# Performance work log

Hardware: AMD Instinct MI355X
Metric: run time of the kernel (lower is better)

## Reference

```python
import jax, jax.numpy as jnp
import numpy as np

B, S, V, NC, CV, CE, WE, KS = 64, 256, 50000, 20, 256, 32, 512, 4


def setup_inputs() -> dict:
    key = jax.random.key(0)
    k1, k2, k3, k4 = jax.random.split(key, 4)
    data = jax.random.randint(k1, (B, S), 0, V, dtype=jnp.int32)
    spelling = jax.random.randint(k2, (V, NC), 0, CV, dtype=jnp.int32)
    char_emb_w = jax.random.normal(k3, (CV, CE), dtype=jnp.float32)
    cnn_w = jax.random.uniform(k4, (WE, CE + 1, KS), dtype=jnp.float32,
                               minval=-0.05, maxval=0.05)
    return {"char_emb_w": char_emb_w, "cnn_w": cnn_w,
            "data": data, "spelling": spelling}


def reference(char_emb_w, cnn_w, data, spelling):
    # spelling gather: [B,S] -> [B,S,NC] char ids -> [B,S,NC,CE] char embeddings
    sp = spelling[data]
    ce = char_emb_w[sp]
    bsz, seq_len, nc, ces = ce.shape
    x = ce.reshape(bsz * seq_len, nc, ces)
    # mode='l2' -> lang bit is 1.0 (would be 0.0 for 'l1')
    lang_bit = jnp.ones((bsz * seq_len, nc, 1), dtype=x.dtype)
    x = jnp.concatenate([x, lang_bit], axis=2).transpose(0, 2, 1)  # [N, CE+1, NC]
    # Conv1d, valid padding, no bias: [N, WE, NC-KS+1]
    y = jax.lax.conv_general_dilated(x, cnn_w, window_strides=(1,),
                                     padding='VALID',
                                     dimension_numbers=('NCH', 'OIH', 'NCH'))
    # MaxPool1d over full remaining length
    word_emb = jnp.max(y, axis=2)  # [N, WE]
    return word_emb.reshape(bsz, seq_len, -1)
```

## Files before the change

### kernel.cpp

```cpp
#include <hip/hip_runtime.h>
#include <hip/hip_bf16.h>
#include <cstdint>

#define NWORDS 16384
#define NCH    20
#define CEDIM  32
#define WEDIM  512
#define WPB    16
#define NBLK   (NWORDS/WPB)

#define AS3 __attribute__((address_space(3)))
#define AS1 __attribute__((address_space(1)))

typedef __attribute__((ext_vector_type(8))) short bf16x8;
typedef __attribute__((ext_vector_type(4))) float f32x4;

__device__ __forceinline__ unsigned short f2bf(float f){
    union { float f; unsigned int u; } v; v.f = f;
    unsigned int u = v.u + 0x7fffu + ((v.u >> 16) & 1u);
    return (unsigned short)(u >> 16);
}

__global__ __launch_bounds__(256) void prep_kernel(const float* __restrict__ cnn,
                                                   const float* __restrict__ cemb,
                                                   unsigned short* __restrict__ wbf2,
                                                   unsigned short* __restrict__ cembbf,
                                                   float* __restrict__ bias){
    int idx = blockIdx.x * 256 + threadIdx.x;
    if (idx < 65536){
        int j  = idx & 7;
        int col= (idx >> 3) & 63;
        int kc = (idx >> 9) & 15;
        int cc = idx >> 13;
        int o  = cc*64 + col;
        int kk = kc*8 + j;
        int i  = kk & 31, k = kk >> 5;
        wbf2[idx] = f2bf(cnn[o*132 + i*4 + k]);
    } else if (idx < 65536 + 257*CEDIM){
        int r = idx - 65536;
        cembbf[r] = (r < 256*CEDIM) ? f2bf(cemb[r]) : (unsigned short)0;
    } else if (idx < 65536 + 257*CEDIM + WEDIM){
        int o = idx - (65536 + 257*CEDIM);
        const float* p = cnn + o*132 + 128;
        bias[o] = p[0] + p[1] + p[2] + p[3];
    }
}

__global__ __attribute__((amdgpu_waves_per_eu(2,2))) __launch_bounds__(256)
void conv_kernel(
    const int* __restrict__ data,
    const int* __restrict__ spelling,
    const unsigned short* __restrict__ cembbf,
    const unsigned short* __restrict__ wbf2,
    const float* __restrict__ bias,
    float* __restrict__ out)
{
    __shared__ __align__(16) unsigned short sW[2][8192];
    __shared__ int scid[WPB*NCH];

    const int tid   = threadIdx.x;
    const int wv    = tid >> 6;
    const int lane  = tid & 63;
    const int lr    = lane & 15, lq = lane >> 4;
    const int wbase = blockIdx.x * WPB;

    {
        const unsigned short* gp0 = wbf2;
        #pragma unroll
        for (int t = 0; t < 4; ++t){
            int slot = wv*4 + t;
            const unsigned short* gp = gp0 + slot*512 + lane*8;
            unsigned short* lp = &sW[0][slot*512];
            __builtin_amdgcn_global_load_lds((const AS1 void*)gp, (AS3 void*)lp, 16, 0, 0);
        }
    }
    for (int s = tid; s < WPB*NCH; s += 256){
        int w = s / NCH, j = s - w*NCH;
        scid[s] = spelling[data[wbase + w]*NCH + j];
    }
    __syncthreads();

    const char* cb = (const char*)cembbf;
    const int lqoff = lq * 16;

    bf16x8 af[4][4];
    #pragma unroll
    for (int mi = 0; mi < 4; ++mi){
        const int* sp = &scid[(wv*4 + mi)*NCH + lr];
        #pragma unroll
        for (int q = 0; q < 4; ++q)
            af[mi][q] = *reinterpret_cast<const bf16x8*>(cb + sp[q]*64 + lqoff);
    }
    bf16x8 axf[4];
    #pragma unroll
    for (int q = 0; q < 4; ++q){
        int ch = (lr < 4) ? scid[(wv*4 + lr)*NCH + 16 + q] : 256;
        axf[q] = *reinterpret_cast<const bf16x8*>(cb + ch*64 + lqoff);
    }

    const float* biasl = bias + lane;

    #pragma unroll 1
    for (int cc = 0; cc < 8; ++cc){
        const int cur = cc & 1, nxt = cur ^ 1;

        if (cc < 7){
            const unsigned short* gp0 = wbf2 + (cc+1)*8192;
            #pragma unroll
            for (int t = 0; t < 4; ++t){
                int slot = wv*4 + t;
                const unsigned short* gp = gp0 + slot*512 + lane*8;
                unsigned short* lp = &sW[nxt][slot*512];
                __builtin_amdgcn_global_load_lds((const AS1 void*)gp, (AS3 void*)lp, 16, 0, 0);
            }
        }

        f32x4 acc[4][4], accX[4];
        {
            f32x4 z = {0.f, 0.f, 0.f, 0.f};
            #pragma unroll
            for (int ni = 0; ni < 4; ++ni){
                accX[ni] = z;
                #pragma unroll
                for (int mi = 0; mi < 4; ++mi) acc[mi][ni] = z;
            }
        }

        #pragma unroll
        for (int q = 0; q < 4; ++q){
            const unsigned short* wl = &sW[cur][(q*4 + lq)*512 + lr*8];
            bf16x8 bb[4];
            #pragma unroll
            for (int ni = 0; ni < 4; ++ni)
                bb[ni] = *reinterpret_cast<const bf16x8*>(wl + ni*128);
            #pragma unroll
            for (int ni = 0; ni < 4; ++ni){
                #pragma unroll
                for (int mi = 0; mi < 4; ++mi)
                    acc[mi][ni] = __builtin_amdgcn_mfma_f32_16x16x32_bf16(
                        af[mi][q], bb[ni], acc[mi][ni], 0, 0, 0);
                accX[ni] = __builtin_amdgcn_mfma_f32_16x16x32_bf16(
                        axf[q], bb[ni], accX[ni], 0, 0, 0);
            }
        }

        float bv = biasl[cc*64];
        #pragma unroll
        for (int mi = 0; mi < 4; ++mi){
            float mred[4];
            #pragma unroll
            for (int ni = 0; ni < 4; ++ni){
                float m = fmaxf(fmaxf(acc[mi][ni][0], acc[mi][ni][1]),
                                fmaxf(acc[mi][ni][2], acc[mi][ni][3]));
                if (lq == 0) m = fmaxf(m, accX[ni][mi]);
                m = fmaxf(m, __shfl_xor(m, 16, 64));
                m = fmaxf(m, __shfl_xor(m, 32, 64));
                mred[ni] = m;
            }
            float mv = (lq == 0) ? mred[0] : (lq == 1) ? mred[1]
                     : (lq == 2) ? mred[2] : mred[3];
            __builtin_nontemporal_store(
                mv + bv, &out[(wbase + wv*4 + mi)*WEDIM + cc*64 + lane]);
        }

        __syncthreads();
    }
}

extern "C" void kernel_launch(void* const* d_in, const int* in_sizes, int n_in,
                              void* d_out, int out_size, void* d_ws, size_t ws_size,
                              hipStream_t stream) {
    const float* cemb     = (const float*)d_in[0];
    const float* cnn      = (const float*)d_in[1];
    const int*   data     = (const int*)d_in[2];
    const int*   spelling = (const int*)d_in[3];
    float* outp = (float*)d_out;

    unsigned short* wbf2   = (unsigned short*)d_ws;
    float*          bias   = (float*)((char*)d_ws + 131072);
    unsigned short* cembbf = (unsigned short*)((char*)d_ws + 133120);

    int prep_items = 65536 + 257*CEDIM + WEDIM;
    prep_kernel<<<dim3((prep_items + 255)/256), dim3(256), 0, stream>>>(cnn, cemb, wbf2, cembbf, bias);
    conv_kernel<<<dim3(NBLK), dim3(256), 0, stream>>>(data, spelling, cembbf, wbf2, bias, outp);
}
```

Measured before the change: 114.1 us.

## Double words per block, stage two weight chunks per barrier, gather spelling directly

Blocks grow from 256 to 512 threads and 32 words, so each weight chunk staged in LDS serves twice as many words. The 8-step loop over output columns becomes 4 phases, each loading two 64-column chunks (32KB per buffer) and issuing half as many barriers. The shared-memory staging of character ids is dropped, and each wave now reads data/spelling directly from global memory into registers. The costs are double the LDS footprint (64KB), which may cut blocks per CU, and redundant per-lane global index loads.

```diff
diff --git a/kernel.cpp b/kernel.cpp
--- a/kernel.cpp
+++ b/kernel.cpp
@@ -6,7 +6,7 @@
 #define NCH    20
 #define CEDIM  32
 #define WEDIM  512
-#define WPB    16
+#define WPB    32
 #define NBLK   (NWORDS/WPB)
 
 #define AS3 __attribute__((address_space(3)))
@@ -46,7 +46,7 @@
     }
 }
 
-__global__ __attribute__((amdgpu_waves_per_eu(2,2))) __launch_bounds__(256)
+__global__ __attribute__((amdgpu_waves_per_eu(2,2))) __launch_bounds__(512)
 void conv_kernel(
     const int* __restrict__ data,
     const int* __restrict__ spelling,
@@ -55,115 +55,114 @@
     const float* __restrict__ bias,
     float* __restrict__ out)
 {
-    __shared__ __align__(16) unsigned short sW[2][8192];
-    __shared__ int scid[WPB*NCH];
+    __shared__ __align__(16) unsigned short sW[2][16384];
 
     const int tid   = threadIdx.x;
     const int wv    = tid >> 6;
     const int lane  = tid & 63;
     const int lr    = lane & 15, lq = lane >> 4;
+    const int lqoff = lq * 16;
     const int wbase = blockIdx.x * WPB;
 
-    {
-        const unsigned short* gp0 = wbf2;
-        #pragma unroll
-        for (int t = 0; t < 4; ++t){
-            int slot = wv*4 + t;
-            const unsigned short* gp = gp0 + slot*512 + lane*8;
-            unsigned short* lp = &sW[0][slot*512];
-            __builtin_amdgcn_global_load_lds((const AS1 void*)gp, (AS3 void*)lp, 16, 0, 0);
-        }
+    #pragma unroll
+    for (int t = 0; t < 4; ++t){
+        int c = t*8 + wv;
+        const unsigned short* gp = wbf2 + c*512 + lane*8;
+        unsigned short* lp = &sW[0][c*512];
+        __builtin_amdgcn_global_load_lds((const AS1 void*)gp, (AS3 void*)lp, 16, 0, 0);
     }
-    for (int s = tid; s < WPB*NCH; s += 256){
-        int w = s / NCH, j = s - w*NCH;
-        scid[s] = spelling[data[wbase + w]*NCH + j];
-    }
-    __syncthreads();
 
     const char* cb = (const char*)cembbf;
-    const int lqoff = lq * 16;
 
     bf16x8 af[4][4];
     #pragma unroll
     for (int mi = 0; mi < 4; ++mi){
-        const int* sp = &scid[(wv*4 + mi)*NCH + lr];
+        int wd = data[wbase + wv*4 + mi];
+        const int* sp = spelling + wd*NCH + lr;
         #pragma unroll
         for (int q = 0; q < 4; ++q)
             af[mi][q] = *reinterpret_cast<const bf16x8*>(cb + sp[q]*64 + lqoff);
     }
     bf16x8 axf[4];
-    #pragma unroll
-    for (int q = 0; q < 4; ++q){
-        int ch = (lr < 4) ? scid[(wv*4 + lr)*NCH + 16 + q] : 256;
-        axf[q] = *reinterpret_cast<const bf16x8*>(cb + ch*64 + lqoff);
+    {
+        int wdx = data[wbase + wv*4 + (lr & 3)];
+        #pragma unroll
+        for (int q = 0; q < 4; ++q){
+            int ch = (lr < 4) ? spelling[wdx*NCH + 16 + q] : 256;
+            axf[q] = *reinterpret_cast<const bf16x8*>(cb + ch*64 + lqoff);
+        }
     }
 
-    const float* biasl = bias + lane;
+    __syncthreads();
 
     #pragma unroll 1
-    for (int cc = 0; cc < 8; ++cc){
-        const int cur = cc & 1, nxt = cur ^ 1;
+    for (int p = 0; p < 4; ++p){
+        const int cur = p & 1, nxt = cur ^ 1;
 
-        if (cc < 7){
-            const unsigned short* gp0 = wbf2 + (cc+1)*8192;
+        if (p < 3){
             #pragma unroll
             for (int t = 0; t < 4; ++t){
-                int slot = wv*4 + t;
-                const unsigned short* gp = gp0 + slot*512 + lane*8;
-                unsigned short* lp = &sW[nxt][slot*512];
+                int c = t*8 + wv;
+                const unsigned short* gp = wbf2 + (p+1)*16384 + c*512 + lane*8;
+                unsigned short* lp = &sW[nxt][c*512];
                 __builtin_amdgcn_global_load_lds((const AS1 void*)gp, (AS3 void*)lp, 16, 0, 0);
             }
         }
 
-        f32x4 acc[4][4], accX[4];
-        {
-            f32x4 z = {0.f, 0.f, 0.f, 0.f};
+        #pragma unroll
+        for (int ccl = 0; ccl < 2; ++ccl){
+            const int cc = p*2 + ccl;
+
+            f32x4 acc[4][4], accX[4];
+            {
+                f32x4 z = {0.f, 0.f, 0.f, 0.f};
+                #pragma unroll
+                for (int ni = 0; ni < 4; ++ni){
+                    accX[ni] = z;
+                    #pragma unroll
+                    for (int mi = 0; mi < 4; ++mi) acc[mi][ni] = z;
+                }
+            }
+
             #pragma unroll
-            for (int ni = 0; ni < 4; ++ni){
-                accX[ni] = z;
+            for (int q = 0; q < 4; ++q){
+                const unsigned short* wl = &sW[cur][ccl*8192 + (q*4 + lq)*512 + lr*8];
+                bf16x8 bb[4];
                 #pragma unroll
-                for (int mi = 0; mi < 4; ++mi) acc[mi][ni] = z;
+                for (int ni = 0; ni < 4; ++ni)
+                    bb[ni] = *reinterpret_cast<const bf16x8*>(wl + ni*128);
+                #pragma unroll
+                for (int ni = 0; ni < 4; ++ni){
+                    #pragma unroll
+                    for (int mi = 0; mi < 4; ++mi)
+                        acc[mi][ni] = __builtin_amdgcn_mfma_f32_16x16x32_bf16(
+                            af[mi][q], bb[ni], acc[mi][ni], 0, 0, 0);
+                    accX[ni] = __builtin_amdgcn_mfma_f32_16x16x32_bf16(
+                            axf[q], bb[ni], accX[ni], 0, 0, 0);
+                }
+            }
+
+            float bv = bias[cc*64 + lane];
+            #pragma unroll
+            for (int mi = 0; mi < 4; ++mi){
+                float mred[4];
+                #pragma unroll
+                for (int ni = 0; ni < 4; ++ni){
+                    float m = fmaxf(fmaxf(acc[mi][ni][0], acc[mi][ni][1]),
+                                    fmaxf(acc[mi][ni][2], acc[mi][ni][3]));
+                    if (lq == 0) m = fmaxf(m, accX[ni][mi]);
+                    m = fmaxf(m, __shfl_xor(m, 16, 64));
+                    m = fmaxf(m, __shfl_xor(m, 32, 64));
+                    mred[ni] = m;
+                }
+                float mv = (lq == 0) ? mred[0] : (lq == 1) ? mred[1]
+                         : (lq == 2) ? mred[2] : mred[3];
+                __builtin_nontemporal_store(
+                    mv + bv, &out[(wbase + wv*4 + mi)*WEDIM + cc*64 + lane]);
             }
         }
 
-        #pragma unroll
-        for (int q = 0; q < 4; ++q){
-            const unsigned short* wl = &sW[cur][(q*4 + lq)*512 + lr*8];
-            bf16x8 bb[4];
-            #pragma unroll
-            for (int ni = 0; ni < 4; ++ni)
-                bb[ni] = *reinterpret_cast<const bf16x8*>(wl + ni*128);
-            #pragma unroll
-            for (int ni = 0; ni < 4; ++ni){
-                #pragma unroll
-                for (int mi = 0; mi < 4; ++mi)
-                    acc[mi][ni] = __builtin_amdgcn_mfma_f32_16x16x32_bf16(
-                        af[mi][q], bb[ni], acc[mi][ni], 0, 0, 0);
-                accX[ni] = __builtin_amdgcn_mfma_f32_16x16x32_bf16(
-                        axf[q], bb[ni], accX[ni], 0, 0, 0);
-            }
-        }
-
-        float bv = biasl[cc*64];
-        #pragma unroll
-        for (int mi = 0; mi < 4; ++mi){
-            float mred[4];
-            #pragma unroll
-            for (int ni = 0; ni < 4; ++ni){
-                float m = fmaxf(fmaxf(acc[mi][ni][0], acc[mi][ni][1]),
-                                fmaxf(acc[mi][ni][2], acc[mi][ni][3]));
-                if (lq == 0) m = fmaxf(m, accX[ni][mi]);
-                m = fmaxf(m, __shfl_xor(m, 16, 64));
-                m = fmaxf(m, __shfl_xor(m, 32, 64));
-                mred[ni] = m;
-            }
-            float mv = (lq == 0) ? mred[0] : (lq == 1) ? mred[1]
-                     : (lq == 2) ? mred[2] : mred[3];
-            __builtin_nontemporal_store(
-                mv + bv, &out[(wbase + wv*4 + mi)*WEDIM + cc*64 + lane]);
-        }
-
-        __syncthreads();
+        if (p < 3) __syncthreads();
     }
 }
 
@@ -182,5 +181,5 @@
 
     int prep_items = 65536 + 257*CEDIM + WEDIM;
     prep_kernel<<<dim3((prep_items + 255)/256), dim3(256), 0, stream>>>(cnn, cemb, wbf2, cembbf, bias);
-    conv_kernel<<<dim3(NBLK), dim3(256), 0, stream>>>(data, spelling, cembbf, wbf2, bias, outp);
+    conv_kernel<<<dim3(NBLK), dim3(512), 0, stream>>>(data, spelling, cembbf, wbf2, bias, outp);
 }
```

Measured after the change: 115.0 us. Within noise of the previous version (+0.8%).

## Restructure MFMA tiling to cut registers, raise occupancy, drop LDS spelling stage

Applied to the files above, without the earlier changes.

The kernel now packs two words per 16-row MFMA tile (8 positions each) and splits each 64-column chunk into two 32-column halves. This shrinks the accumulator set from 20 f32x4 to 10 so the kernel can run at 3 waves per EU instead of being pinned to 2. Spelling ids are read straight from global memory per lane instead of being staged in LDS, which removes a sync and the scid array. The last-iteration barrier is also skipped. The costs are a slightly different max-reduction pattern, more redundant global index loads per lane, and possibly worse MFMA back-to-back scheduling within each half.

```diff
diff --git a/kernel.cpp b/kernel.cpp
--- a/kernel.cpp
+++ b/kernel.cpp
@@ -46,7 +46,7 @@
     }
 }
 
-__global__ __attribute__((amdgpu_waves_per_eu(2,2))) __launch_bounds__(256)
+__global__ __attribute__((amdgpu_waves_per_eu(3))) __launch_bounds__(256)
 void conv_kernel(
     const int* __restrict__ data,
     const int* __restrict__ spelling,
@@ -56,114 +56,114 @@
     float* __restrict__ out)
 {
     __shared__ __align__(16) unsigned short sW[2][8192];
-    __shared__ int scid[WPB*NCH];
 
     const int tid   = threadIdx.x;
     const int wv    = tid >> 6;
     const int lane  = tid & 63;
     const int lr    = lane & 15, lq = lane >> 4;
+    const int lqoff = lq * 16;
     const int wbase = blockIdx.x * WPB;
 
-    {
-        const unsigned short* gp0 = wbf2;
+    #pragma unroll
+    for (int t = 0; t < 4; ++t){
+        int slot = wv*4 + t;
+        const unsigned short* gp = wbf2 + slot*512 + lane*8;
+        unsigned short* lp = &sW[0][slot*512];
+        __builtin_amdgcn_global_load_lds((const AS1 void*)gp, (AS3 void*)lp, 16, 0, 0);
+    }
+
+    const char* cb = (const char*)cembbf;
+
+    bf16x8 af[2][2][4];
+    #pragma unroll
+    for (int p = 0; p < 2; ++p){
+        int wd = data[wbase + wv*4 + 2*p + (lr >> 3)];
+        const int* sp = spelling + wd*NCH;
         #pragma unroll
-        for (int t = 0; t < 4; ++t){
-            int slot = wv*4 + t;
-            const unsigned short* gp = gp0 + slot*512 + lane*8;
-            unsigned short* lp = &sW[0][slot*512];
-            __builtin_amdgcn_global_load_lds((const AS1 void*)gp, (AS3 void*)lp, 16, 0, 0);
+        for (int h = 0; h < 2; ++h){
+            int b = h*8 + (lr & 7);
+            #pragma unroll
+            for (int q = 0; q < 4; ++q)
+                af[p][h][q] = *reinterpret_cast<const bf16x8*>(cb + sp[b+q]*64 + lqoff);
         }
     }
-    for (int s = tid; s < WPB*NCH; s += 256){
-        int w = s / NCH, j = s - w*NCH;
-        scid[s] = spelling[data[wbase + w]*NCH + j];
-    }
-    __syncthreads();
-
-    const char* cb = (const char*)cembbf;
-    const int lqoff = lq * 16;
-
-    bf16x8 af[4][4];
-    #pragma unroll
-    for (int mi = 0; mi < 4; ++mi){
-        const int* sp = &scid[(wv*4 + mi)*NCH + lr];
+    bf16x8 axf[4];
+    {
+        bool valid = (lr & 7) < 2;
+        int wloc = 2*(lr & 7) + (lr >> 3);
+        int wdx = data[wbase + wv*4 + (valid ? wloc : 0)];
         #pragma unroll
-        for (int q = 0; q < 4; ++q)
-            af[mi][q] = *reinterpret_cast<const bf16x8*>(cb + sp[q]*64 + lqoff);
-    }
-    bf16x8 axf[4];
-    #pragma unroll
-    for (int q = 0; q < 4; ++q){
-        int ch = (lr < 4) ? scid[(wv*4 + lr)*NCH + 16 + q] : 256;
-        axf[q] = *reinterpret_cast<const bf16x8*>(cb + ch*64 + lqoff);
+        for (int q = 0; q < 4; ++q){
+            int ch = valid ? spelling[wdx*NCH + 16 + q] : 256;
+            axf[q] = *reinterpret_cast<const bf16x8*>(cb + ch*64 + lqoff);
+        }
     }
 
-    const float* biasl = bias + lane;
+    __syncthreads();
 
     #pragma unroll 1
     for (int cc = 0; cc < 8; ++cc){
         const int cur = cc & 1, nxt = cur ^ 1;
 
         if (cc < 7){
-            const unsigned short* gp0 = wbf2 + (cc+1)*8192;
             #pragma unroll
             for (int t = 0; t < 4; ++t){
                 int slot = wv*4 + t;
-                const unsigned short* gp = gp0 + slot*512 + lane*8;
+                const unsigned short* gp = wbf2 + (cc+1)*8192 + slot*512 + lane*8;
                 unsigned short* lp = &sW[nxt][slot*512];
                 __builtin_amdgcn_global_load_lds((const AS1 void*)gp, (AS3 void*)lp, 16, 0, 0);
             }
         }
 
-        f32x4 acc[4][4], accX[4];
-        {
-            f32x4 z = {0.f, 0.f, 0.f, 0.f};
+        #pragma unroll
+        for (int n = 0; n < 2; ++n){
+            f32x4 acc[8], accX[2];
+            {
+                f32x4 z = {0.f, 0.f, 0.f, 0.f};
+                #pragma unroll
+                for (int i = 0; i < 8; ++i) acc[i] = z;
+                accX[0] = z; accX[1] = z;
+            }
+
             #pragma unroll
-            for (int ni = 0; ni < 4; ++ni){
-                accX[ni] = z;
+            for (int q = 0; q < 4; ++q){
+                const unsigned short* wl = &sW[cur][(q*4 + lq)*512 + (n*32 + lr)*8];
+                bf16x8 bb0 = *reinterpret_cast<const bf16x8*>(wl);
+                bf16x8 bb1 = *reinterpret_cast<const bf16x8*>(wl + 128);
                 #pragma unroll
-                for (int mi = 0; mi < 4; ++mi) acc[mi][ni] = z;
+                for (int p = 0; p < 2; ++p)
+                    #pragma unroll
+                    for (int h = 0; h < 2; ++h){
+                        acc[(p*2+h)*2+0] = __builtin_amdgcn_mfma_f32_16x16x32_bf16(
+                            af[p][h][q], bb0, acc[(p*2+h)*2+0], 0, 0, 0);
+                        acc[(p*2+h)*2+1] = __builtin_amdgcn_mfma_f32_16x16x32_bf16(
+                            af[p][h][q], bb1, acc[(p*2+h)*2+1], 0, 0, 0);
+                    }
+                accX[0] = __builtin_amdgcn_mfma_f32_16x16x32_bf16(axf[q], bb0, accX[0], 0, 0, 0);
+                accX[1] = __builtin_amdgcn_mfma_f32_16x16x32_bf16(axf[q], bb1, accX[1], 0, 0, 0);
+            }
+
+            #pragma unroll
+            for (int p = 0; p < 2; ++p){
+                float m[2];
+                #pragma unroll
+                for (int nl = 0; nl < 2; ++nl){
+                    f32x4 a0 = acc[(p*2+0)*2+nl];
+                    f32x4 a1 = acc[(p*2+1)*2+nl];
+                    float v = fmaxf(fmaxf(fmaxf(a0[0], a0[1]), fmaxf(a0[2], a0[3])),
+                                    fmaxf(fmaxf(a1[0], a1[1]), fmaxf(a1[2], a1[3])));
+                    if ((lq & 1) == 0) v = fmaxf(v, accX[nl][p]);
+                    v = fmaxf(v, __shfl_xor(v, 16, 64));
+                    m[nl] = v;
+                }
+                int col  = cc*64 + n*32 + (lq & 1)*16 + lr;
+                int word = wbase + wv*4 + 2*p + (lq >> 1);
+                float mv = (lq & 1) ? m[1] : m[0];
+                __builtin_nontemporal_store(mv + bias[col], &out[word*WEDIM + col]);
             }
         }
 
-        #pragma unroll
-        for (int q = 0; q < 4; ++q){
-            const unsigned short* wl = &sW[cur][(q*4 + lq)*512 + lr*8];
-            bf16x8 bb[4];
-            #pragma unroll
-            for (int ni = 0; ni < 4; ++ni)
-                bb[ni] = *reinterpret_cast<const bf16x8*>(wl + ni*128);
-            #pragma unroll
-            for (int ni = 0; ni < 4; ++ni){
-                #pragma unroll
-                for (int mi = 0; mi < 4; ++mi)
-                    acc[mi][ni] = __builtin_amdgcn_mfma_f32_16x16x32_bf16(
-                        af[mi][q], bb[ni], acc[mi][ni], 0, 0, 0);
-                accX[ni] = __builtin_amdgcn_mfma_f32_16x16x32_bf16(
-                        axf[q], bb[ni], accX[ni], 0, 0, 0);
-            }
-        }
-
-        float bv = biasl[cc*64];
-        #pragma unroll
-        for (int mi = 0; mi < 4; ++mi){
-            float mred[4];
-            #pragma unroll
-            for (int ni = 0; ni < 4; ++ni){
-                float m = fmaxf(fmaxf(acc[mi][ni][0], acc[mi][ni][1]),
-                                fmaxf(acc[mi][ni][2], acc[mi][ni][3]));
-                if (lq == 0) m = fmaxf(m, accX[ni][mi]);
-                m = fmaxf(m, __shfl_xor(m, 16, 64));
-                m = fmaxf(m, __shfl_xor(m, 32, 64));
-                mred[ni] = m;
-            }
-            float mv = (lq == 0) ? mred[0] : (lq == 1) ? mred[1]
-                     : (lq == 2) ? mred[2] : mred[3];
-            __builtin_nontemporal_store(
-                mv + bv, &out[(wbase + wv*4 + mi)*WEDIM + cc*64 + lane]);
-        }
-
-        __syncthreads();
+        if (cc < 7) __syncthreads();
     }
 }
 
```

Result: faster. 107.7 us (-5.6%).
